# Kernel tuning notes

Measured on AMD Instinct MI355X. Metric: run time of the kernel, lower is better.

Reference implementation:

```python
import jax, jax.numpy as jnp
from jax import lax
import numpy as np

# Constants from the source module
DMIN, DMAX = 1.0, 50.0
NUM_PLANES = 8            # number of depth-hypothesis planes
FOCAL = 307.98 // 4.0     # focal // downsample (stride-4 features) -> 76.0 px

B, C, H, W = 4, 64, 96, 320


def _plane_shifts(dtype):
    # reciprocal (inverse-depth) spaced hypothesis planes: d_i = 1/disp_i
    disp = jnp.linspace(1.0 / DMAX, 1.0 / DMIN, NUM_PLANES, dtype=dtype)
    return (FOCAL * disp).astype(dtype)  # per-plane vertical pixel shift f/d


def _warp_vertical(x, shifts):
    """Bilinear vertical homography warp of x [B,C,H,W] for each shift.
    Returns [B,D,C,H,W]; out-of-image samples are zero."""
    Bb, Cc, Hh, Ww = x.shape
    D = shifts.shape[0]
    y = jnp.arange(Hh, dtype=x.dtype)                 # [H]
    y_src = y[None, :] + shifts[:, None]              # [D,H]
    y0 = jnp.floor(y_src)
    w = (y_src - y0)                                  # bilinear weight [D,H]
    y0i = y0.astype(jnp.int32)
    y1i = y0i + 1
    v0 = ((y0i >= 0) & (y0i < Hh)).astype(x.dtype)    # validity masks [D,H]
    v1 = ((y1i >= 0) & (y1i < Hh)).astype(x.dtype)
    y0c = jnp.clip(y0i, 0, Hh - 1).reshape(-1)        # [D*H]
    y1c = jnp.clip(y1i, 0, Hh - 1).reshape(-1)
    # gather rows: [B,C,D*H,W] -> [B,C,D,H,W]
    g0 = jnp.take(x, y0c, axis=2).reshape(Bb, Cc, D, Hh, Ww)
    g1 = jnp.take(x, y1c, axis=2).reshape(Bb, Cc, D, Hh, Ww)
    wb = w[None, None, :, :, None]
    out = (1.0 - wb) * v0[None, None, :, :, None] * g0 + wb * v1[None, None, :, :, None] * g1
    return jnp.transpose(out, (0, 2, 1, 3, 4))        # [B,D,C,H,W]


def _depth_recip_conv(x, Wk, b):
    """Warp to each hypothesis plane, conv each, max-project over planes."""
    Bb, Cc, Hh, Ww = x.shape
    warped = _warp_vertical(x, _plane_shifts(x.dtype))        # [B,D,C,H,W]
    D = warped.shape[1]
    xr = warped.reshape(Bb * D, Cc, Hh, Ww)
    y = lax.conv_general_dilated(xr, Wk, window_strides=(1, 1), padding='SAME',
                                 dimension_numbers=('NCHW', 'OIHW', 'NCHW'))
    Co = Wk.shape[0]
    y = y.reshape(Bb, D, Co, Hh, Ww).max(axis=1)              # max-projection
    return y + b[None, :, None, None]


def setup_inputs() -> dict:
    key = jax.random.key(0)
    k1, k2, k3, k4, k5 = jax.random.split(key, 5)
    fan = C * 9
    return {
        'x': jax.random.normal(k1, (B, C, H, W), dtype=jnp.float32),
        'W1': jax.random.normal(k2, (C, C, 3, 3), dtype=jnp.float32) / np.sqrt(fan),
        'b1': jax.random.normal(k3, (C,), dtype=jnp.float32) * 0.01,
        'W2': jax.random.normal(k4, (C, C, 3, 3), dtype=jnp.float32) / np.sqrt(fan),
        'b2': jax.random.normal(k5, (C,), dtype=jnp.float32) * 0.01,
    }


def reference(x, W1, b1, W2, b2):
    x = jax.nn.relu(_depth_recip_conv(x, W1, b1))
    x = jax.nn.relu(_depth_recip_conv(x, W2, b2))
    return x
```

## Files before the change

kernel.cpp:

```cpp
#include <hip/hip_runtime.h>
#include <math.h>

#define HH 96
#define WW 320
#define NP 8

typedef _Float16 half8_t  __attribute__((ext_vector_type(8)));
typedef _Float16 half4_t  __attribute__((ext_vector_type(4)));
typedef float    floatx16 __attribute__((ext_vector_type(16)));

struct ShiftInfo {
    int   s0[NP];
    float wa[NP];
    float wb[NP];
    int   rows[16];
};

__device__ __forceinline__ void gl_lds16(const _Float16* g, _Float16* l) {
    __builtin_amdgcn_global_load_lds(
        (const __attribute__((address_space(1))) void*)g,
        (__attribute__((address_space(3))) void*)l, 16, 0, 0);
}

__global__ __launch_bounds__(256) void prep_kernel(
    const float* __restrict__ X, const float* __restrict__ W1,
    const float* __restrict__ W2, _Float16* __restrict__ Xt,
    _Float16* __restrict__ Wf)
{
    __shared__ __align__(16) _Float16 Ls[64 * 163];
    const int bx = blockIdx.x, t = threadIdx.x;
    if (bx < 768) {
        const int r = bx >> 1, xh = bx & 1;
        const int y = r % HH, b = r / HH;
        const int xbase = xh * 160;
        for (int u = t; u < 64 * 40; u += 256) {
            int ci = u / 40;
            int xi = (u - ci * 40) * 4;
            float4 v = *(const float4*)&X[((size_t)(b * 64 + ci) * HH + y) * WW + xbase + xi];
            half4_t hv = { (_Float16)v.x, (_Float16)v.y, (_Float16)v.z, (_Float16)v.w };
            *(half4_t*)&Ls[ci * 163 + xi] = hv;
        }
        __syncthreads();
        const int ci8 = t & 7, xg = t >> 3;
        for (int it = 0; it < 5; ++it) {
            int x = xg + 32 * it;
            half8_t o;
#pragma unroll
            for (int j = 0; j < 8; ++j) o[j] = Ls[(ci8 * 8 + j) * 163 + x];
            *(half8_t*)&Xt[((size_t)(b * HH + y) * WW + xbase + x) * 64 + ci8 * 8] = o;
        }
    } else {
        const int k = bx - 768;
        const int layer = k / 9, pos = k - layer * 9;
        const float* Ws = layer ? W2 : W1;
        _Float16* Wd = Wf + layer * 36864 + pos * 4096;
        for (int u = t; u < 4096; u += 256) {
            int mt  = u >> 11;
            int ks  = (u >> 9) & 3;
            int i31 = (u >> 4) & 31;
            int h   = (u >> 3) & 1;
            int j   = u & 7;
            int co  = mt * 32 + i31;
            int ci  = ks * 16 + h * 8 + j;
            Wd[u] = (_Float16)Ws[((size_t)co * 64 + ci) * 9 + pos];
        }
    }
}

template<int MODE, int NPOS>
__device__ __forceinline__ void conv_core(
    const _Float16* __restrict__ Xs, _Float16* __restrict__ Wl,
    const _Float16* __restrict__ Wg, int w, int i31, int h, int t,
    floatx16 (&acc)[2][2])
{
    int xsw[3], xbase[3];
#pragma unroll
    for (int kx = 0; kx < 3; ++kx) {
        int x = i31 + kx;
        xsw[kx]   = x & 7;
        xbase[kx] = x * 64;
    }
    const int rowb  = w * (66 * 64);
    const int wv    = t >> 6, l = t & 63;
    const int wfrag = i31 * 16 + h * 8;

#pragma unroll
    for (int p = 0; p < NPOS; ++p) {
        if (p + 1 < NPOS) {
#pragma unroll
            for (int j = 0; j < 2; ++j) {
                int ch = wv * 2 + j;
                gl_lds16(Wg + (p + 1) * 4096 + ch * 512 + l * 8,
                         Wl + ((p + 1) & 1) * 4096 + ch * 512);
            }
        }
        const int ky = p / 3, kx = p - ky * 3;
        const _Float16* wb = Wl + (p & 1) * 4096 + wfrag;
        half8_t fw0[4], fw1[4], fx0[4], fx1[4];
#pragma unroll
        for (int ks = 0; ks < 4; ++ks) {
            fw0[ks] = *(const half8_t*)(wb + ks * 512);
            fw1[ks] = *(const half8_t*)(wb + ks * 512 + 2048);
            const int c8  = ks * 2 + h;
            const int off = rowb + ky * (66 * 64) + xbase[kx] + ((c8 ^ xsw[kx]) * 8);
            fx0[ks] = *(const half8_t*)(Xs + off);
            fx1[ks] = *(const half8_t*)(Xs + off + 32 * 64);
        }
#pragma unroll
        for (int ks = 0; ks < 4; ++ks) {
            if (MODE == 1) {
                acc[0][0] = __builtin_amdgcn_mfma_f32_32x32x16_f16(fx0[ks], fw0[ks], acc[0][0], 0, 0, 0);
                acc[0][1] = __builtin_amdgcn_mfma_f32_32x32x16_f16(fx0[ks], fw1[ks], acc[0][1], 0, 0, 0);
                acc[1][0] = __builtin_amdgcn_mfma_f32_32x32x16_f16(fx1[ks], fw0[ks], acc[1][0], 0, 0, 0);
                acc[1][1] = __builtin_amdgcn_mfma_f32_32x32x16_f16(fx1[ks], fw1[ks], acc[1][1], 0, 0, 0);
            } else {
                acc[0][0] = __builtin_amdgcn_mfma_f32_32x32x16_f16(fw0[ks], fx0[ks], acc[0][0], 0, 0, 0);
                acc[0][1] = __builtin_amdgcn_mfma_f32_32x32x16_f16(fw0[ks], fx1[ks], acc[0][1], 0, 0, 0);
                acc[1][0] = __builtin_amdgcn_mfma_f32_32x32x16_f16(fw1[ks], fx0[ks], acc[1][0], 0, 0, 0);
                acc[1][1] = __builtin_amdgcn_mfma_f32_32x32x16_f16(fw1[ks], fx1[ks], acc[1][1], 0, 0, 0);
            }
        }
        if (p + 1 < NPOS) __syncthreads();
    }
}

template<int MODE>
__global__ __launch_bounds__(256, 2) void conv_kernel(
    const _Float16* __restrict__ Xt, const _Float16* __restrict__ Wfl,
    _Float16* __restrict__ OutE, _Float16* __restrict__ OutT, ShiftInfo si)
{
    __shared__ __align__(16) _Float16 Xs[6 * 66 * 64];
    __shared__ __align__(16) _Float16 Wl[2 * 4096];
    const int xt = blockIdx.x, rg = blockIdx.y, b = blockIdx.z;
    const bool top = rg >= 24;
    const int trg = rg - 24;
    const int x0 = xt * 64;
    const int t  = threadIdx.x;

    int grow[6];
#pragma unroll
    for (int r = 0; r < 6; ++r)
        grow[r] = top ? ((r < 4) ? si.rows[trg * 4 + r] : -1) : rg * 4 + r;

    {
        const int wv = t >> 6, l = t & 63;
#pragma unroll
        for (int j = 0; j < 2; ++j) {
            int ch = wv * 2 + j;
            gl_lds16(Wfl + ch * 512 + l * 8, Wl + ch * 512);
        }
    }

    {
        const int w = t >> 6, l = t & 63;
#pragma unroll
        for (int j = 0; j < 12; ++j) {
            int k = w + 4 * j;
            int r = k >> 3, c = k & 7;
            if ((unsigned)grow[r] < HH) {
                int x  = 1 + 8 * c + (l >> 3);
                int c8 = (l & 7) ^ (x & 7);
                const _Float16* g =
                    &Xt[((size_t)(b * HH + grow[r]) * WW + (x0 - 1 + x)) * 64 + c8 * 8];
                gl_lds16(g, &Xs[(r * 66 + 1 + 8 * c) * 64]);
            }
        }
    }

#pragma unroll
    for (int r = 0; r < 6; ++r) {
        if ((unsigned)grow[r] >= HH) {
            for (int u = t; u < 66 * 8; u += 256) {
                float4 zz = make_float4(0.f, 0.f, 0.f, 0.f);
                *(float4*)&Xs[r * (66 * 64) + u * 8] = zz;
            }
        }
    }

    if (t < 96) {
        int r  = t >> 4, hx = (t >> 3) & 1, c8 = t & 7;
        int x  = hx ? 65 : 0;
        int gx = x0 - 1 + x;
        float4 v = make_float4(0.f, 0.f, 0.f, 0.f);
        if ((unsigned)grow[r] < HH && (unsigned)gx < WW)
            v = *(const float4*)&Xt[((size_t)(b * HH + grow[r]) * WW + gx) * 64 + c8 * 8];
        *(float4*)&Xs[(r * 66 + x) * 64 + ((c8 ^ (x & 7)) * 8)] = v;
    }
    __syncthreads();

    const int l = t & 63, w = t >> 6;
    const int i31 = l & 31, h = l >> 5;

    floatx16 acc[2][2];
#pragma unroll
    for (int a = 0; a < 2; ++a)
#pragma unroll
        for (int c = 0; c < 2; ++c)
            acc[a][c] = (floatx16){0.f,0.f,0.f,0.f, 0.f,0.f,0.f,0.f,
                                   0.f,0.f,0.f,0.f, 0.f,0.f,0.f,0.f};

    if (top) conv_core<MODE, 3>(Xs, Wl, Wfl, w, i31, h, t, acc);
    else     conv_core<MODE, 9>(Xs, Wl, Wfl, w, i31, h, t, acc);

    const int OH = top ? 16 : HH;
    const int om = top ? (trg * 4 + w) : (rg * 4 + w);
    _Float16* Out = top ? OutT : OutE;
#pragma unroll
    for (int a = 0; a < 2; ++a)
#pragma unroll
        for (int c = 0; c < 2; ++c)
#pragma unroll
            for (int r = 0; r < 16; ++r) {
                int dm = (r & 3) + 8 * (r >> 2) + 4 * h;
                if (MODE == 1) {
                    int x  = x0 + a * 32 + dm;
                    int co = c * 32 + i31;
                    Out[((size_t)(b * OH + om) * WW + x) * 64 + co] = (_Float16)acc[a][c][r];
                } else {
                    int co = a * 32 + dm;
                    int x  = x0 + c * 32 + i31;
                    Out[((size_t)(b * 64 + co) * OH + om) * WW + x] = (_Float16)acc[a][c][r];
                }
            }
}

__global__ __launch_bounds__(256) void blend1_kernel(
    const _Float16* __restrict__ Cb, const _Float16* __restrict__ T,
    const float* __restrict__ bias, _Float16* __restrict__ Xt2, ShiftInfo si)
{
    __shared__ __align__(16) _Float16 Cs[96 * 64];
    __shared__ __align__(16) _Float16 Ts[16 * 64];
    const int x0 = blockIdx.x, b = blockIdx.y, t = threadIdx.x;
    const half8_t z = {0,0,0,0,0,0,0,0};

    {
        const int w = t >> 6, l = t & 63;
        const int c8 = l & 7;
#pragma unroll
        for (int j = 0; j < 3; ++j) {
            int k = w + 4 * j;
            int row = 8 * k + (l >> 3);
            gl_lds16(&Cb[((size_t)(b * HH + row) * WW + x0) * 64 + c8 * 8],
                     &Cs[k * 512]);
        }
        if (w < 2) {
            int row = 8 * w + (l >> 3);
            gl_lds16(&T[((size_t)(b * 16 + row) * WW + x0) * 64 + c8 * 8],
                     &Ts[w * 512]);
        }
    }
    __syncthreads();

    const int co8 = t & 7, yt = t >> 3;
    half8_t bv;
#pragma unroll
    for (int j = 0; j < 8; ++j) bv[j] = (_Float16)bias[co8 * 8 + j];

    const int y0 = yt * 3;
    half8_t cur[NP];
#pragma unroll
    for (int d = 0; d < NP; ++d) {
        int r = y0 + si.s0[d] - 1;
        cur[d] = (r < HH) ? *(const half8_t*)&Cs[r * 64 + co8 * 8] : z;
    }
    for (int y = y0; y < y0 + 3; ++y) {
        half8_t m = z;
#pragma unroll
        for (int d = 0; d < NP; ++d) {
            int r1 = y + si.s0[d];
            half8_t v1 = (r1 < HH) ? *(const half8_t*)&Cs[r1 * 64 + co8 * 8] : z;
            half8_t v0 = cur[d];
            cur[d] = v1;
            _Float16 a = (_Float16)si.wa[d], wg = (_Float16)si.wb[d];
            half8_t p;
            if (y == 0) {
                half8_t t0 = *(const half8_t*)&Ts[(2 * d) * 64 + co8 * 8];
                half8_t t1 = *(const half8_t*)&Ts[(2 * d + 1) * 64 + co8 * 8];
                p = a * (v0 - t0) + wg * (v1 - t1);
            } else {
                p = a * v0 + wg * v1;
            }
            m = (d == 0) ? p : __builtin_elementwise_max(m, p);
        }
        half8_t o = __builtin_elementwise_max(m + bv, z);
        *(half8_t*)&Xt2[((size_t)(b * HH + y) * WW + x0) * 64 + co8 * 8] = o;
    }
}

__global__ __launch_bounds__(256) void blend2_kernel(
    const _Float16* __restrict__ Cb, const _Float16* __restrict__ T,
    const float* __restrict__ bias, float* __restrict__ Out, ShiftInfo si)
{
    __shared__ __align__(16) _Float16 Cs[96 * 64];
    __shared__ __align__(16) _Float16 Ts[16 * 64];
    const int task = blockIdx.x, t = threadIdx.x;
    const int xt = task % 5;
    const int rem = task / 5;
    const int co = rem & 63;
    const int b  = rem >> 6;
    const int x0 = xt * 64;
    const half8_t z = {0,0,0,0,0,0,0,0};

    {
        const int w = t >> 6, l = t & 63;
        const int x8 = l & 7;
#pragma unroll
        for (int j = 0; j < 3; ++j) {
            int k = w + 4 * j;
            int row = 8 * k + (l >> 3);
            gl_lds16(&Cb[((size_t)(b * 64 + co) * HH + row) * WW + x0 + x8 * 8],
                     &Cs[k * 512]);
        }
        if (w < 2) {
            int row = 8 * w + (l >> 3);
            gl_lds16(&T[((size_t)(b * 64 + co) * 16 + row) * WW + x0 + x8 * 8],
                     &Ts[w * 512]);
        }
    }
    __syncthreads();

    const int x8 = t & 7, yt = t >> 3;
    const float bvf = bias[co];
    const int y0 = yt * 3;

    half8_t cur[NP];
#pragma unroll
    for (int d = 0; d < NP; ++d) {
        int r = y0 + si.s0[d] - 1;
        cur[d] = (r < HH) ? *(const half8_t*)&Cs[r * 64 + x8 * 8] : z;
    }
    for (int y = y0; y < y0 + 3; ++y) {
        half8_t m = z;
#pragma unroll
        for (int d = 0; d < NP; ++d) {
            int r1 = y + si.s0[d];
            half8_t v1 = (r1 < HH) ? *(const half8_t*)&Cs[r1 * 64 + x8 * 8] : z;
            half8_t v0 = cur[d];
            cur[d] = v1;
            _Float16 a = (_Float16)si.wa[d], wg = (_Float16)si.wb[d];
            half8_t p;
            if (y == 0) {
                half8_t t0 = *(const half8_t*)&Ts[(2 * d) * 64 + x8 * 8];
                half8_t t1 = *(const half8_t*)&Ts[(2 * d + 1) * 64 + x8 * 8];
                p = a * (v0 - t0) + wg * (v1 - t1);
            } else {
                p = a * v0 + wg * v1;
            }
            m = (d == 0) ? p : __builtin_elementwise_max(m, p);
        }
        float4 o0, o1;
        o0.x = fmaxf((float)m[0] + bvf, 0.f);
        o0.y = fmaxf((float)m[1] + bvf, 0.f);
        o0.z = fmaxf((float)m[2] + bvf, 0.f);
        o0.w = fmaxf((float)m[3] + bvf, 0.f);
        o1.x = fmaxf((float)m[4] + bvf, 0.f);
        o1.y = fmaxf((float)m[5] + bvf, 0.f);
        o1.z = fmaxf((float)m[6] + bvf, 0.f);
        o1.w = fmaxf((float)m[7] + bvf, 0.f);
        float* op = Out + ((size_t)(b * 64 + co) * HH + y) * WW + x0 + x8 * 8;
        *(float4*)op = o0;
        *(float4*)(op + 4) = o1;
    }
}

extern "C" void kernel_launch(void* const* d_in, const int* in_sizes, int n_in,
                              void* d_out, int out_size, void* d_ws, size_t ws_size,
                              hipStream_t stream) {
    const float* x  = (const float*)d_in[0];
    const float* W1 = (const float*)d_in[1];
    const float* b1 = (const float*)d_in[2];
    const float* W2 = (const float*)d_in[3];
    const float* b2 = (const float*)d_in[4];
    float* out = (float*)d_out;

    _Float16* Xt1 = (_Float16*)d_ws;
    _Float16* Cb  = Xt1 + 7864320;
    _Float16* T   = Cb  + 7864320;
    _Float16* Wf  = T   + 1310720;
    _Float16* Xt2 = (_Float16*)d_out;

    ShiftInfo si;
    for (int d = 0; d < NP; ++d) {
        double disp = 0.02 + d * (0.98 / 7.0);
        double sh   = 76.0 * disp;
        int s0      = (int)floor(sh);
        double w    = sh - (double)s0;
        si.s0[d] = s0;
        si.wa[d] = (float)(1.0 - w);
        si.wb[d] = (float)w;
        si.rows[2 * d]     = s0 - 1;
        si.rows[2 * d + 1] = s0;
    }

    prep_kernel<<<dim3(786), 256, 0, stream>>>(x, W1, W2, Xt1, Wf);

    conv_kernel<1><<<dim3(5, 28, 4), 256, 0, stream>>>(Xt1, Wf, Cb, T, si);
    blend1_kernel<<<dim3(320, 4), 256, 0, stream>>>(Cb, T, b1, Xt2, si);

    conv_kernel<2><<<dim3(5, 28, 4), 256, 0, stream>>>(Xt2, Wf + 36864, Cb, T, si);
    blend2_kernel<<<dim3(1280), 256, 0, stream>>>(Cb, T, b2, out, si);
}
```

Measured before the change: 77.44 us.

## Fold top-row partial convs into main conv blocks, shrink grid

Drops the separate grid rows that computed the 16 extra top-row partial (ky-only) convolutions. Instead, the first 16 row-group blocks each compute one extra row after the main conv, with only wave 0 doing the 3-position MFMA work using register-held weights. This removes 80 small-work blocks per conv launch and their tail imbalance. The cost is extra serialized work with three idle waves in those blocks, plus more register pressure from the 24 weight fragments.

```diff
diff --git a/kernel.cpp b/kernel.cpp
--- a/kernel.cpp
+++ b/kernel.cpp
@@ -67,7 +67,7 @@
     }
 }
 
-template<int MODE, int NPOS>
+template<int MODE>
 __device__ __forceinline__ void conv_core(
     const _Float16* __restrict__ Xs, _Float16* __restrict__ Wl,
     const _Float16* __restrict__ Wg, int w, int i31, int h, int t,
@@ -85,8 +85,8 @@
     const int wfrag = i31 * 16 + h * 8;
 
 #pragma unroll
-    for (int p = 0; p < NPOS; ++p) {
-        if (p + 1 < NPOS) {
+    for (int p = 0; p < 9; ++p) {
+        if (p + 1 < 9) {
 #pragma unroll
             for (int j = 0; j < 2; ++j) {
                 int ch = wv * 2 + j;
@@ -120,7 +120,7 @@
                 acc[1][1] = __builtin_amdgcn_mfma_f32_32x32x16_f16(fw1[ks], fx1[ks], acc[1][1], 0, 0, 0);
             }
         }
-        if (p + 1 < NPOS) __syncthreads();
+        if (p + 1 < 9) __syncthreads();
     }
 }
 
@@ -132,18 +132,16 @@
     __shared__ __align__(16) _Float16 Xs[6 * 66 * 64];
     __shared__ __align__(16) _Float16 Wl[2 * 4096];
     const int xt = blockIdx.x, rg = blockIdx.y, b = blockIdx.z;
-    const bool top = rg >= 24;
-    const int trg = rg - 24;
     const int x0 = xt * 64;
     const int t  = threadIdx.x;
+    const int wv = t >> 6, l = t & 63;
+    const int i31 = l & 31, h = l >> 5;
 
     int grow[6];
 #pragma unroll
-    for (int r = 0; r < 6; ++r)
-        grow[r] = top ? ((r < 4) ? si.rows[trg * 4 + r] : -1) : rg * 4 + r;
+    for (int r = 0; r < 6; ++r) grow[r] = rg * 4 + r;
 
     {
-        const int wv = t >> 6, l = t & 63;
 #pragma unroll
         for (int j = 0; j < 2; ++j) {
             int ch = wv * 2 + j;
@@ -152,10 +150,9 @@
     }
 
     {
-        const int w = t >> 6, l = t & 63;
 #pragma unroll
         for (int j = 0; j < 12; ++j) {
-            int k = w + 4 * j;
+            int k = wv + 4 * j;
             int r = k >> 3, c = k & 7;
             if ((unsigned)grow[r] < HH) {
                 int x  = 1 + 8 * c + (l >> 3);
@@ -188,9 +185,6 @@
     }
     __syncthreads();
 
-    const int l = t & 63, w = t >> 6;
-    const int i31 = l & 31, h = l >> 5;
-
     floatx16 acc[2][2];
 #pragma unroll
     for (int a = 0; a < 2; ++a)
@@ -199,29 +193,116 @@
             acc[a][c] = (floatx16){0.f,0.f,0.f,0.f, 0.f,0.f,0.f,0.f,
                                    0.f,0.f,0.f,0.f, 0.f,0.f,0.f,0.f};
 
-    if (top) conv_core<MODE, 3>(Xs, Wl, Wfl, w, i31, h, t, acc);
-    else     conv_core<MODE, 9>(Xs, Wl, Wfl, w, i31, h, t, acc);
-
-    const int OH = top ? 16 : HH;
-    const int om = top ? (trg * 4 + w) : (rg * 4 + w);
-    _Float16* Out = top ? OutT : OutE;
-#pragma unroll
-    for (int a = 0; a < 2; ++a)
-#pragma unroll
-        for (int c = 0; c < 2; ++c)
-#pragma unroll
-            for (int r = 0; r < 16; ++r) {
-                int dm = (r & 3) + 8 * (r >> 2) + 4 * h;
-                if (MODE == 1) {
-                    int x  = x0 + a * 32 + dm;
-                    int co = c * 32 + i31;
-                    Out[((size_t)(b * OH + om) * WW + x) * 64 + co] = (_Float16)acc[a][c][r];
-                } else {
-                    int co = a * 32 + dm;
-                    int x  = x0 + c * 32 + i31;
-                    Out[((size_t)(b * 64 + co) * OH + om) * WW + x] = (_Float16)acc[a][c][r];
+    conv_core<MODE>(Xs, Wl, Wfl, wv, i31, h, t, acc);
+
+    {
+        const int om = rg * 4 + wv;
+#pragma unroll
+        for (int a = 0; a < 2; ++a)
+#pragma unroll
+            for (int c = 0; c < 2; ++c)
+#pragma unroll
+                for (int r = 0; r < 16; ++r) {
+                    int dm = (r & 3) + 8 * (r >> 2) + 4 * h;
+                    if (MODE == 1) {
+                        int x  = x0 + a * 32 + dm;
+                        int co = c * 32 + i31;
+                        OutE[((size_t)(b * HH + om) * WW + x) * 64 + co] = (_Float16)acc[a][c][r];
+                    } else {
+                        int co = a * 32 + dm;
+                        int x  = x0 + c * 32 + i31;
+                        OutE[((size_t)(b * 64 + co) * HH + om) * WW + x] = (_Float16)acc[a][c][r];
+                    }
                 }
-            }
+    }
+
+    if (rg < 16) {
+        const int tr = rg;
+        const int trow = si.rows[tr];
+        __syncthreads();
+
+        half8_t fwp0[12], fwp1[12];
+        if (wv == 0) {
+#pragma unroll
+            for (int p = 0; p < 3; ++p)
+#pragma unroll
+                for (int ks = 0; ks < 4; ++ks) {
+                    const _Float16* wp = Wfl + p * 4096 + ks * 512 + i31 * 16 + h * 8;
+                    fwp0[p * 4 + ks] = *(const half8_t*)(wp);
+                    fwp1[p * 4 + ks] = *(const half8_t*)(wp + 2048);
+                }
+        }
+
+#pragma unroll
+        for (int j = 0; j < 2; ++j) {
+            int c = wv * 2 + j;
+            int x = 1 + 8 * c + (l >> 3);
+            int c8 = (l & 7) ^ (x & 7);
+            gl_lds16(&Xt[((size_t)(b * HH + trow) * WW + (x0 - 1 + x)) * 64 + c8 * 8],
+                     &Xs[(1 + 8 * c) * 64]);
+        }
+        if (t < 16) {
+            int hx = t >> 3, c8 = t & 7;
+            int x  = hx ? 65 : 0;
+            int gx = x0 - 1 + x;
+            float4 v = make_float4(0.f, 0.f, 0.f, 0.f);
+            if ((unsigned)gx < WW)
+                v = *(const float4*)&Xt[((size_t)(b * HH + trow) * WW + gx) * 64 + c8 * 8];
+            *(float4*)&Xs[x * 64 + ((c8 ^ (x & 7)) * 8)] = v;
+        }
+        __syncthreads();
+
+        if (wv == 0) {
+            floatx16 a2[2][2];
+#pragma unroll
+            for (int a = 0; a < 2; ++a)
+#pragma unroll
+                for (int c = 0; c < 2; ++c)
+                    a2[a][c] = (floatx16){0.f,0.f,0.f,0.f, 0.f,0.f,0.f,0.f,
+                                          0.f,0.f,0.f,0.f, 0.f,0.f,0.f,0.f};
+#pragma unroll
+            for (int p = 0; p < 3; ++p) {
+                const int kx = p;
+                const int x = i31 + kx;
+#pragma unroll
+                for (int ks = 0; ks < 4; ++ks) {
+                    const int c8  = ks * 2 + h;
+                    const int off = x * 64 + ((c8 ^ (x & 7)) * 8);
+                    half8_t fx0v = *(const half8_t*)(Xs + off);
+                    half8_t fx1v = *(const half8_t*)(Xs + off + 32 * 64);
+                    half8_t w0 = fwp0[p * 4 + ks], w1 = fwp1[p * 4 + ks];
+                    if (MODE == 1) {
+                        a2[0][0] = __builtin_amdgcn_mfma_f32_32x32x16_f16(fx0v, w0, a2[0][0], 0, 0, 0);
+                        a2[0][1] = __builtin_amdgcn_mfma_f32_32x32x16_f16(fx0v, w1, a2[0][1], 0, 0, 0);
+                        a2[1][0] = __builtin_amdgcn_mfma_f32_32x32x16_f16(fx1v, w0, a2[1][0], 0, 0, 0);
+                        a2[1][1] = __builtin_amdgcn_mfma_f32_32x32x16_f16(fx1v, w1, a2[1][1], 0, 0, 0);
+                    } else {
+                        a2[0][0] = __builtin_amdgcn_mfma_f32_32x32x16_f16(w0, fx0v, a2[0][0], 0, 0, 0);
+                        a2[0][1] = __builtin_amdgcn_mfma_f32_32x32x16_f16(w0, fx1v, a2[0][1], 0, 0, 0);
+                        a2[1][0] = __builtin_amdgcn_mfma_f32_32x32x16_f16(w1, fx0v, a2[1][0], 0, 0, 0);
+                        a2[1][1] = __builtin_amdgcn_mfma_f32_32x32x16_f16(w1, fx1v, a2[1][1], 0, 0, 0);
+                    }
+                }
+            }
+#pragma unroll
+            for (int a = 0; a < 2; ++a)
+#pragma unroll
+                for (int c = 0; c < 2; ++c)
+#pragma unroll
+                    for (int r = 0; r < 16; ++r) {
+                        int dm = (r & 3) + 8 * (r >> 2) + 4 * h;
+                        if (MODE == 1) {
+                            int x  = x0 + a * 32 + dm;
+                            int co = c * 32 + i31;
+                            OutT[((size_t)(b * 16 + tr) * WW + x) * 64 + co] = (_Float16)a2[a][c][r];
+                        } else {
+                            int co = a * 32 + dm;
+                            int x  = x0 + c * 32 + i31;
+                            OutT[((size_t)(b * 64 + co) * 16 + tr) * WW + x] = (_Float16)a2[a][c][r];
+                        }
+                    }
+        }
+    }
 }
 
 __global__ __launch_bounds__(256) void blend1_kernel(
@@ -394,9 +475,9 @@
 
     prep_kernel<<<dim3(786), 256, 0, stream>>>(x, W1, W2, Xt1, Wf);
 
-    conv_kernel<1><<<dim3(5, 28, 4), 256, 0, stream>>>(Xt1, Wf, Cb, T, si);
+    conv_kernel<1><<<dim3(5, 24, 4), 256, 0, stream>>>(Xt1, Wf, Cb, T, si);
     blend1_kernel<<<dim3(320, 4), 256, 0, stream>>>(Cb, T, b1, Xt2, si);
 
-    conv_kernel<2><<<dim3(5, 28, 4), 256, 0, stream>>>(Xt2, Wf + 36864, Cb, T, si);
+    conv_kernel<2><<<dim3(5, 24, 4), 256, 0, stream>>>(Xt2, Wf + 36864, Cb, T, si);
     blend2_kernel<<<dim3(1280), 256, 0, stream>>>(Cb, T, b2, out, si);
 }
```

Result: no change. 75.93 us (-2.0%).
